# Performance work log

Measured on AMD Instinct MI355X. Metric: run time of the kernel, lower is better.

## Reference

```python
import jax, jax.numpy as jnp
import numpy as np

U, I, G = 200000, 100000, 10000
D = 64
LAYERS = 3
E_HG = 3_000_000
E_GI = 2_000_000
B = 8192


def setup_inputs() -> dict:
    key = jax.random.key(0)
    ks = jax.random.split(key, 20)
    n_hg = U + G
    n_gi = G + I
    xav = lambda k, shape: (jax.random.normal(k, shape, jnp.float32) * 0.05)
    inp = {
        "user_inputs": jax.random.randint(ks[0], (B,), 0, U),
        "pos_groups": jax.random.randint(ks[1], (B,), 0, G),
        "neg_groups": jax.random.randint(ks[2], (B,), 0, G),
        # hypergraph propagation matrix (normalized-adjacency-like values)
        "hg_rows": jax.random.randint(ks[3], (E_HG,), 0, n_hg),
        "hg_cols": jax.random.randint(ks[4], (E_HG,), 0, n_hg),
        "hg_vals": jax.random.uniform(ks[5], (E_HG,), jnp.float32) / 16.0,
        # group-item bipartite graph (one LightGCN hop)
        "gi_rows": jax.random.randint(ks[6], (E_GI,), 0, n_gi),
        "gi_cols": jax.random.randint(ks[7], (E_GI,), 0, n_gi),
        "gi_vals": jax.random.uniform(ks[8], (E_GI,), jnp.float32) / 16.0,
        # dense group-group overlap matrix
        "gg_graph": jax.random.uniform(ks[9], (G, G), jnp.float32) / float(G),
        # learned parameters
        "user_emb": xav(ks[10], (U, D)),
        "item_emb": xav(ks[11], (I, D)),
        "group_emb": xav(ks[12], (G, D)),
        "hyper_w": xav(ks[13], (D, 1)),
        "hyper_b": jnp.zeros((1,), jnp.float32),
        "lightgcn_w": xav(ks[14], (D, 1)),
        "lightgcn_b": jnp.zeros((1,), jnp.float32),
        "overlap_w": xav(ks[15], (D, 1)),
        "overlap_b": jnp.zeros((1,), jnp.float32),
    }
    return inp


def spmm(rows, cols, vals, x, n):
    # sparse(n,n) @ x : gather cols, scale, scatter-add into rows
    return jax.ops.segment_sum(vals[:, None] * x[cols], rows, num_segments=n)


def reference(user_inputs, pos_groups, neg_groups,
              hg_rows, hg_cols, hg_vals,
              gi_rows, gi_cols, gi_vals,
              gg_graph,
              user_emb, item_emb, group_emb,
              hyper_w, hyper_b, lightgcn_w, lightgcn_b, overlap_w, overlap_b):
    # --- hypergraph branch: layered SpMM + mean over (layers+1) views ---
    hg = jnp.concatenate([user_emb, group_emb], axis=0)  # [U+G, D]
    acc = hg
    cur = hg
    for _ in range(LAYERS):
        cur = spmm(hg_rows, hg_cols, hg_vals, cur, U + G)
        acc = acc + cur
    hg_mean = acc / float(LAYERS + 1)
    hg_users = hg_mean[:U]   # [U, D]
    hg_groups = hg_mean[U:]  # [G, D]

    # --- lightgcn branch: one SpMM hop over group-item graph ---
    gi = jnp.concatenate([group_emb, item_emb], axis=0)  # [G+I, D]
    gi = spmm(gi_rows, gi_cols, gi_vals, gi, G + I)
    gi_groups = gi[:G]

    # --- overlap branch: dense group-group propagation ---
    gg = gg_graph @ group_emb  # [G, D]

    # --- gated multi-view fusion ---
    sig = jax.nn.sigmoid
    hyper_coef = sig(hg_groups @ hyper_w + hyper_b)      # [G, 1]
    lightgcn_coef = sig(gi_groups @ lightgcn_w + lightgcn_b)
    overlap_coef = sig(gg @ overlap_w + overlap_b)
    groups_final = hyper_coef * hg_groups + lightgcn_coef * gi_groups + overlap_coef * gg
    users_final = hg_users

    return (users_final[user_inputs], groups_final[pos_groups], groups_final[neg_groups],
            user_emb[user_inputs], group_emb[pos_groups], group_emb[neg_groups])
```

## Files before the change

kernel.cpp:

```cpp
#include <hip/hip_runtime.h>
#include <hip/hip_bf16.h>

#define U_N 200000
#define I_N 100000
#define G_N 10000
#define B_N 8192
#define NHG (U_N + G_N)
#define GG_K 10000
#define GG_KC 313
#define GG_STRIPES 157
#define GG_SPLIT 8

#define BUCK_SHIFT 8
#define BUCK_ROWS 256
#define NBUCK 821
#define ACHUNK 12288

typedef __attribute__((ext_vector_type(8))) short bf16x8;
typedef __attribute__((ext_vector_type(4))) float f32x4;
typedef __attribute__((ext_vector_type(8))) float f32x8;
typedef __attribute__((ext_vector_type(8))) unsigned short us8;

static __device__ __forceinline__ float sigmoidf_(float x) {
    return 1.0f / (1.0f + __expf(-x));
}

static __device__ __forceinline__ unsigned bfc(float x) {
    unsigned u = __float_as_uint(x);
    return (u + 0x7fffu + ((u >> 16) & 1u)) >> 16;
}
static __device__ __forceinline__ float bsf(unsigned short u) {
    return __uint_as_float((unsigned)u << 16);
}

__global__ void k_phase1(const float* __restrict__ ge, short* __restrict__ Bfrag,
                         int* __restrict__ cursor, int cap, int bfB) {
    int bx = blockIdx.x;
    if (bx < bfB) {
        int t = bx * 256 + threadIdx.x;
        int l = t & 63;
        int ct = (t >> 6) & 3;
        int kc = t >> 8;
        int j = ct * 16 + (l & 15);
        int kb = kc * 32 + (l >> 4) * 8;
        bf16x8 pack;
#pragma unroll
        for (int e = 0; e < 8; ++e) {
            int k = kb + e;
            float f = (k < GG_K) ? ge[(size_t)k * 64 + j] : 0.f;
            pack[e] = (short)bfc(f);
        }
        *(bf16x8*)(Bfrag + (size_t)t * 8) = pack;
        return;
    }
    int b = (bx - bfB) * 256 + threadIdx.x;
    if (b < NBUCK) cursor[b] = b * cap;
}


static __device__ __forceinline__ void bscatter_body(const int* __restrict__ rows,
                                                     const int* __restrict__ cols,
                                                     const float* __restrict__ vals,
                                                     int* __restrict__ cursor,
                                                     int2* __restrict__ bpair,
                                                     int nE, int cap, int blk) {
    __shared__ int h[NBUCK];
    __shared__ int base[NBUCK];
    for (int i = threadIdx.x; i < NBUCK; i += 256) h[i] = 0;
    __syncthreads();
    int s = blk * ACHUNK;
    int end = s + ACHUNK; if (end > nE) end = nE;
    for (int e = s + threadIdx.x; e < end; e += 256)
        atomicAdd(&h[rows[e] >> BUCK_SHIFT], 1);
    __syncthreads();
    for (int i = threadIdx.x; i < NBUCK; i += 256) {
        int c = h[i];
        base[i] = c ? atomicAdd(&cursor[i], c) : 0;
        h[i] = 0;
    }
    __syncthreads();
    for (int e = s + threadIdx.x; e < end; e += 256) {
        int r = rows[e];
        int b = r >> BUCK_SHIFT;
        int pos = base[b] + atomicAdd(&h[b], 1);
        if (pos < (b + 1) * cap)
            bpair[pos] = make_int2(((r & (BUCK_ROWS - 1)) << 24) | cols[e],
                                   __float_as_int(vals[e]));
    }
}

static __device__ __forceinline__ void gg_mfma_body(const float* __restrict__ A,
                                                    const short* __restrict__ Bfrag,
                                                    float* __restrict__ part, int blk) {
    const int stripe = blk % GG_STRIPES;
    const int ks = blk / GG_STRIPES;
    const int w = threadIdx.x >> 6;
    const int l = threadIdx.x & 63;
    const int r0w = stripe * 64 + w * 16;
    int arow_i = r0w + (l & 15);
    if (arow_i > GG_K - 1) arow_i = GG_K - 1;
    const float* arow = A + (size_t)arow_i * GG_K;
    const int kg8 = (l >> 4) * 8;
    const int c0 = (ks == 0) ? 0 : 40 + 39 * (ks - 1);
    const int c1 = c0 + ((ks == 0) ? 40 : 39);
    f32x4 acc0 = {0.f, 0.f, 0.f, 0.f}, acc1 = acc0, acc2 = acc0, acc3 = acc0;
    for (int kc = c0; kc < c1; ++kc) {
        const int kbase = kc * 32 + kg8;
        bf16x8 af;
        if (kc != GG_KC - 1) {
            const float4 a0 = *(const float4*)(arow + kbase);
            const float4 a1 = *(const float4*)(arow + kbase + 4);
            af[0] = (short)bfc(a0.x); af[1] = (short)bfc(a0.y);
            af[2] = (short)bfc(a0.z); af[3] = (short)bfc(a0.w);
            af[4] = (short)bfc(a1.x); af[5] = (short)bfc(a1.y);
            af[6] = (short)bfc(a1.z); af[7] = (short)bfc(a1.w);
        } else {
#pragma unroll
            for (int e = 0; e < 8; ++e) {
                int k = kbase + e;
                af[e] = (short)bfc((k < GG_K) ? arow[k] : 0.f);
            }
        }
        const bf16x8* bp = (const bf16x8*)(Bfrag + (size_t)kc * 4 * 64 * 8);
        bf16x8 b0 = bp[0 * 64 + l];
        bf16x8 b1 = bp[1 * 64 + l];
        bf16x8 b2 = bp[2 * 64 + l];
        bf16x8 b3 = bp[3 * 64 + l];
        acc0 = __builtin_amdgcn_mfma_f32_16x16x32_bf16(af, b0, acc0, 0, 0, 0);
        acc1 = __builtin_amdgcn_mfma_f32_16x16x32_bf16(af, b1, acc1, 0, 0, 0);
        acc2 = __builtin_amdgcn_mfma_f32_16x16x32_bf16(af, b2, acc2, 0, 0, 0);
        acc3 = __builtin_amdgcn_mfma_f32_16x16x32_bf16(af, b3, acc3, 0, 0, 0);
    }
    float* po = part + (size_t)ks * GG_K * 64;
    const int orow0 = r0w + (l >> 4) * 4;
    const int ocol = l & 15;
#pragma unroll
    for (int reg = 0; reg < 4; ++reg) {
        int orow = orow0 + reg;
        if (orow < GG_K) {
            float* q = po + (size_t)orow * 64 + ocol;
            q[0]  = acc0[reg];
            q[16] = acc1[reg];
            q[32] = acc2[reg];
            q[48] = acc3[reg];
        }
    }
}

__global__ __launch_bounds__(256) void k_phase2(
    const int* __restrict__ rows, const int* __restrict__ cols,
    const float* __restrict__ vals, int* __restrict__ cursor,
    int2* __restrict__ bpair, int nE, int cap,
    const float* __restrict__ A, const short* __restrict__ Bfrag,
    float* __restrict__ part,
    const float4* __restrict__ ue4, const float4* __restrict__ ge4,
    ushort4* __restrict__ out4, const int* __restrict__ ui,
    float* __restrict__ ua, float* __restrict__ grp_acc, float* __restrict__ gi_out,
    int bsB, int ggB, int cvtB, int uaB, int gaB) {
    int bx = blockIdx.x;
    if (bx < bsB) { bscatter_body(rows, cols, vals, cursor, bpair, nE, cap, bx); return; }
    bx -= bsB;
    if (bx < ggB) { gg_mfma_body(A, Bfrag, part, bx); return; }
    bx -= ggB;
    if (bx < cvtB) {
        int i = bx * 256 + threadIdx.x;
        float4 f = (i < U_N * 16) ? ue4[i] : ge4[i - U_N * 16];
        ushort4 o;
        o.x = (unsigned short)bfc(f.x);
        o.y = (unsigned short)bfc(f.y);
        o.z = (unsigned short)bfc(f.z);
        o.w = (unsigned short)bfc(f.w);
        out4[i] = o;
        return;
    }
    bx -= cvtB;
    if (bx < uaB) {
        int idx = bx * 256 + threadIdx.x;
        int b = idx >> 6, d = idx & 63;
        ua[idx] = ((const float*)ue4)[(size_t)ui[b] * 64 + d];
        return;
    }
    bx -= uaB;
    if (bx < gaB) {
        int idx = bx * 256 + threadIdx.x;
        grp_acc[idx] = ((const float*)ge4)[idx];
        return;
    }
    bx -= gaB;
    int idx = bx * 256 + threadIdx.x;
    gi_out[idx] = 0.f;
}


static __device__ __forceinline__ void bcsr_body(const int* __restrict__ cursor,
                                                 const int2* __restrict__ bpair,
                                                 int2* __restrict__ ep,
                                                 int* __restrict__ rp, int* __restrict__ cnt,
                                                 int cap, int b) {
    __shared__ int hist[256];
    __shared__ int sc[256];
    const int tid = threadIdx.x;
    const int s = b * cap;
    int e_ = cursor[b];
    if (e_ > s + cap) e_ = s + cap;
    hist[tid] = 0;
    __syncthreads();
    for (int i = s + tid; i < e_; i += 256)
        atomicAdd(&hist[((unsigned)bpair[i].x) >> 24], 1);
    __syncthreads();
    int v = hist[tid];
    sc[tid] = v;
    __syncthreads();
    for (int off = 1; off < 256; off <<= 1) {
        int t = (tid >= off) ? sc[tid - off] : 0;
        __syncthreads();
        if (tid >= off) sc[tid] += t;
        __syncthreads();
    }
    int excl = sc[tid] - v;
    int gr = (b << BUCK_SHIFT) + tid;
    if (gr < NHG) { rp[gr] = s + excl; cnt[gr] = v; }
    hist[tid] = excl;
    __syncthreads();
    for (int i = s + tid; i < e_; i += 256) {
        int2 p = bpair[i];
        unsigned pk = (unsigned)p.x;
        int pos = atomicAdd(&hist[pk >> 24], 1);
        ep[s + pos] = make_int2((int)(pk & 0xFFFFFFu), p.y);
    }
}

static __device__ __forceinline__ void gi_body(const int* __restrict__ rows,
                                               const int* __restrict__ cols,
                                               const float* __restrict__ vals,
                                               const float* __restrict__ ge,
                                               const float* __restrict__ ie,
                                               float* __restrict__ out, int nE,
                                               int blk, int nblk) {
    int lane = threadIdx.x & 63;
    long wslot = (long)blk * 4 + (threadIdx.x >> 6);
    const long nslots = (long)nblk * 4;
    for (long base = wslot * 64; base < nE; base += nslots * 64) {
        long e = base + lane;
        int r = (e < nE) ? rows[e] : 0x7fffffff;
        bool ok = (r < G_N);
        int c = 0;
        float v = 0.f;
        if (ok) { c = cols[e]; v = vals[e]; }
        unsigned long long mask = __ballot(ok);
        while (mask) {
            int srcl = __ffsll(mask) - 1;
            mask &= mask - 1;
            int rr = __shfl(r, srcl, 64);
            int cc = __shfl(c, srcl, 64);
            float vv = __shfl(v, srcl, 64);
            const float* sp = (cc < G_N) ? (ge + (size_t)cc * 64) : (ie + (size_t)(cc - G_N) * 64);
            atomicAdd(&out[(size_t)rr * 64 + lane], vv * sp[lane]);
        }
    }
}

__global__ __launch_bounds__(256) void k_phase3(const int* __restrict__ cursor,
                                                const int2* __restrict__ bpair,
                                                int2* __restrict__ ep,
                                                int* __restrict__ rp, int* __restrict__ cnt,
                                                int cap,
                                                const int* __restrict__ grows,
                                                const int* __restrict__ gcols,
                                                const float* __restrict__ gvals,
                                                const float* __restrict__ ge,
                                                const float* __restrict__ ie,
                                                float* __restrict__ gi_out, int gnE, int giB) {
    if (blockIdx.x < NBUCK)
        bcsr_body(cursor, bpair, ep, rp, cnt, cap, blockIdx.x);
    else
        gi_body(grows, gcols, gvals, ge, ie, gi_out, gnE, blockIdx.x - NBUCK, giB);
}


static __device__ __forceinline__ void spmm_row8(const int2* __restrict__ ep, int s, int n,
                                                 const us8* __restrict__ x16,
                                                 int sub, f32x8& acc) {
#pragma unroll
    for (int t = 0; t < 8; ++t) acc[t] = 0.f;
    for (int i = 0; i < n; i += 8) {
        int2 e[8];
#pragma unroll
        for (int j = 0; j < 8; ++j) {
            int k = i + j;
            int kk = (k < n) ? k : n - 1;
            e[j] = ep[s + kk];
            if (k >= n) { e[j].y = 0; e[j].x = 0; }
        }
        us8 xv[8];
#pragma unroll
        for (int j = 0; j < 8; ++j)
            xv[j] = x16[(size_t)e[j].x * 8 + sub];
#pragma unroll
        for (int j = 0; j < 8; ++j) {
            float v = __int_as_float(e[j].y);
#pragma unroll
            for (int t = 0; t < 8; ++t) acc[t] += v * bsf(xv[j][t]);
        }
    }
}

__global__ void k_spmm8(const int* __restrict__ rp, const int* __restrict__ cnt,
                        const int2* __restrict__ ep, const us8* __restrict__ x16,
                        us8* __restrict__ out16, float* __restrict__ grp_acc,
                        const int* __restrict__ ui, float* __restrict__ usr_acc,
                        int spmmBlocks) {
    if (blockIdx.x >= spmmBlocks) {
        int idx = (blockIdx.x - spmmBlocks) * 256 + threadIdx.x;
        int b = idx >> 3, d = idx & 7;
        us8 u = x16[(size_t)ui[b] * 8 + d];
        f32x8* g = (f32x8*)usr_acc + ((size_t)b * 8 + d);
        f32x8 t = *g;
#pragma unroll
        for (int j = 0; j < 8; ++j) t[j] += bsf(u[j]);
        *g = t;
        return;
    }
    int wid = threadIdx.x >> 6;
    int lane = threadIdx.x & 63;
    int slot = lane >> 3, sub = lane & 7;
    int r = blockIdx.x * 32 + wid * 8 + slot;
    bool active = (r < NHG);
    int rr = active ? r : NHG - 1;
    int s = rp[rr];
    int n = active ? cnt[rr] : 0;
    f32x8 a;
    spmm_row8(ep, s, n, x16, sub, a);
    if (active) {
        us8 o;
#pragma unroll
        for (int j = 0; j < 8; ++j) o[j] = (unsigned short)bfc(a[j]);
        out16[(size_t)r * 8 + sub] = o;
        if (r >= U_N) {
            f32x8* g = (f32x8*)grp_acc + ((size_t)(r - U_N) * 8 + sub);
            f32x8 t = *g;
#pragma unroll
            for (int j = 0; j < 8; ++j) t[j] += a[j];
            *g = t;
        }
    }
}

__global__ void k_spmm8_final(const int* __restrict__ rp, const int* __restrict__ cnt,
                              const int2* __restrict__ ep, const us8* __restrict__ x16,
                              const int* __restrict__ ui,
                              float* __restrict__ grp_acc, float* __restrict__ usr_acc,
                              int taskBlocks) {
    if (blockIdx.x >= taskBlocks) {
        int idx = (blockIdx.x - taskBlocks) * 256 + threadIdx.x;
        int b = idx >> 3, d = idx & 7;
        us8 u = x16[(size_t)ui[b] * 8 + d];
        f32x8* g = (f32x8*)usr_acc + ((size_t)b * 8 + d);
        f32x8 t = *g;
#pragma unroll
        for (int j = 0; j < 8; ++j) t[j] += bsf(u[j]);
        *g = t;
        return;
    }
    int wid = threadIdx.x >> 6;
    int lane = threadIdx.x & 63;
    int slot = lane >> 3, sub = lane & 7;
    int t = blockIdx.x * 32 + wid * 8 + slot;
    bool active = (t < G_N + B_N);
    int tt = active ? t : 0;
    int r = (tt < G_N) ? (U_N + tt) : ui[tt - G_N];
    int s = rp[r];
    int n = active ? cnt[r] : 0;
    f32x8 a;
    spmm_row8(ep, s, n, x16, sub, a);
    if (active) {
        f32x8* g = (tt < G_N) ? ((f32x8*)grp_acc + ((size_t)tt * 8 + sub))
                              : ((f32x8*)usr_acc + ((size_t)(tt - G_N) * 8 + sub));
        f32x8 v = *g;
#pragma unroll
        for (int j = 0; j < 8; ++j) v[j] += a[j];
        *g = v;
    }
}


__global__ void k_gather_fin(const int* __restrict__ ui, const int* __restrict__ pg,
                             const int* __restrict__ ng, const float* __restrict__ ua,
                             const float* __restrict__ ga, const float* __restrict__ gi_out,
                             const float* __restrict__ gg_part,
                             const float* __restrict__ hw, const float* __restrict__ hb,
                             const float* __restrict__ lw, const float* __restrict__ lb,
                             const float* __restrict__ ow, const float* __restrict__ ob,
                             const float* __restrict__ ue, const float* __restrict__ ge,
                             float* __restrict__ out) {
    int wid = threadIdx.x >> 6, lane = threadIdx.x & 63;
    int b = blockIdx.x * 4 + wid;
    const int S = B_N * 64;
    int u = ui[b], p = pg[b], q = ng[b];
    int idx = b * 64 + lane;
    out[idx]         = ua[idx] * 0.25f;
    out[3 * S + idx] = ue[(size_t)u * 64 + lane];
    out[4 * S + idx] = ge[(size_t)p * 64 + lane];
    out[5 * S + idx] = ge[(size_t)q * 64 + lane];
    const size_t SS = (size_t)G_N * 64;
    float hwv = hw[lane], lwv = lw[lane], owv = ow[lane];
    float hb0 = hb[0], lb0 = lb[0], ob0 = ob[0];
#pragma unroll
    for (int which = 0; which < 2; ++which) {
        int g = which ? q : p;
        size_t o = (size_t)g * 64 + lane;
        float hgv = ga[o] * 0.25f;
        float giv = gi_out[o];
        float ggv = 0.f;
#pragma unroll
        for (int k = 0; k < GG_SPLIT; ++k) ggv += gg_part[k * SS + o];
        float d1 = hgv * hwv, d2 = giv * lwv, d3 = ggv * owv;
#pragma unroll
        for (int off2 = 32; off2; off2 >>= 1) {
            d1 += __shfl_xor(d1, off2, 64);
            d2 += __shfl_xor(d2, off2, 64);
            d3 += __shfl_xor(d3, off2, 64);
        }
        float val = sigmoidf_(d1 + hb0) * hgv + sigmoidf_(d2 + lb0) * giv
                  + sigmoidf_(d3 + ob0) * ggv;
        out[(which ? 2 * S : S) + idx] = val;
    }
}

extern "C" void kernel_launch(void* const* d_in, const int* in_sizes, int n_in,
                              void* d_out, int out_size, void* d_ws, size_t ws_size,
                              hipStream_t stream) {
    const int*   ui        = (const int*)d_in[0];
    const int*   pg        = (const int*)d_in[1];
    const int*   ng        = (const int*)d_in[2];
    const int*   hg_rows   = (const int*)d_in[3];
    const int*   hg_cols   = (const int*)d_in[4];
    const float* hg_vals   = (const float*)d_in[5];
    const int*   gi_rows   = (const int*)d_in[6];
    const int*   gi_cols   = (const int*)d_in[7];
    const float* gi_vals   = (const float*)d_in[8];
    const float* gg_graph  = (const float*)d_in[9];
    const float* user_emb  = (const float*)d_in[10];
    const float* item_emb  = (const float*)d_in[11];
    const float* group_emb = (const float*)d_in[12];
    const float* hyper_w   = (const float*)d_in[13];
    const float* hyper_b   = (const float*)d_in[14];
    const float* lgcn_w    = (const float*)d_in[15];
    const float* lgcn_b    = (const float*)d_in[16];
    const float* ovl_w     = (const float*)d_in[17];
    const float* ovl_b     = (const float*)d_in[18];
    const int E_HG = in_sizes[3];
    const int E_GI = in_sizes[6];

    const int nblkA = (E_HG + ACHUNK - 1) / ACHUNK;
    int cap = (E_HG + NBUCK - 1) / NBUCK;
    cap = cap + cap / 4 + 64;
    cap = (cap + 63) & ~63;

    char* ws = (char*)d_ws;
    size_t off = 0;
    auto alloc = [&](size_t bytes) -> char* {
        char* p = ws + off;
        off += (bytes + 255) & ~(size_t)255;
        return p;
    };
    int*   cursor  = (int*)alloc((size_t)NBUCK * 4);
    int2*  bpair   = (int2*)alloc((size_t)NBUCK * cap * 8);
    int2*  ep      = (int2*)alloc((size_t)NBUCK * cap * 8 + 1024);
    int*   rp      = (int*)alloc((size_t)NHG * 4);
    int*   cnt     = (int*)alloc((size_t)NHG * 4);
    __hip_bfloat16* curA = (__hip_bfloat16*)alloc((size_t)NHG * 64 * 2);
    __hip_bfloat16* curB = (__hip_bfloat16*)alloc((size_t)NHG * 64 * 2);
    float* grp_acc = (float*)alloc((size_t)G_N * 64 * 4);
    float* gi_out  = (float*)alloc((size_t)G_N * 64 * 4);
    float* usr_acc = (float*)alloc((size_t)B_N * 64 * 4);
    short* Bfrag   = (short*)alloc((size_t)GG_KC * 4 * 64 * 8 * 2);
    float* gg_part = (float*)alloc((size_t)GG_SPLIT * GG_K * 64 * 4);
    (void)ws_size; (void)n_in; (void)out_size;

    k_phase1<<<GG_KC + 4, 256, 0, stream>>>(group_emb, Bfrag, cursor, cap, GG_KC);

    const int ggB  = GG_STRIPES * GG_SPLIT;
    const int cvtB = (NHG * 16) / 256;
    const int uaB  = (B_N * 64) / 256;
    const int gaB  = (G_N * 64) / 256;
    const int gzB  = (G_N * 64) / 256;
    k_phase2<<<nblkA + ggB + cvtB + uaB + gaB + gzB, 256, 0, stream>>>(
        hg_rows, hg_cols, hg_vals, cursor, bpair, E_HG, cap,
        gg_graph, Bfrag, gg_part,
        (const float4*)user_emb, (const float4*)group_emb, (ushort4*)curB, ui,
        usr_acc, grp_acc, gi_out, nblkA, ggB, cvtB, uaB, gaB);

    const int giB = 2048;
    k_phase3<<<NBUCK + giB, 256, 0, stream>>>(cursor, bpair, ep, rp, cnt, cap,
                                              gi_rows, gi_cols, gi_vals,
                                              group_emb, item_emb, gi_out, E_GI, giB);

    const int spmmB = (NHG + 31) / 32;
    const int uaExt = (B_N * 8) / 256;

    k_spmm8<<<spmmB, 256, 0, stream>>>(rp, cnt, ep, (const us8*)curB,
                                       (us8*)curA, grp_acc, nullptr, nullptr, spmmB);
    k_spmm8<<<spmmB + uaExt, 256, 0, stream>>>(rp, cnt, ep, (const us8*)curA,
                                               (us8*)curB, grp_acc, ui, usr_acc, spmmB);
    const int taskB = (G_N + B_N + 31) / 32;
    k_spmm8_final<<<taskB + uaExt, 256, 0, stream>>>(rp, cnt, ep, (const us8*)curB, ui,
                                                     grp_acc, usr_acc, taskB);

    k_gather_fin<<<B_N / 4, 256, 0, stream>>>(ui, pg, ng, usr_acc, grp_acc, gi_out, gg_part,
                                              hyper_w, hyper_b, lgcn_w, lgcn_b, ovl_w, ovl_b,
                                              user_emb, group_emb, (float*)d_out);
}
```

Before: 416.9 us.

## Replace atomic bucket cursors with per-block histogram plus global exclusive scan

```diff
diff --git a/kernel.cpp b/kernel.cpp
--- a/kernel.cpp
+++ b/kernel.cpp
@@ -33,59 +33,110 @@
     return __uint_as_float((unsigned)u << 16);
 }
 
-__global__ void k_phase1(const float* __restrict__ ge, short* __restrict__ Bfrag,
-                         int* __restrict__ cursor, int cap, int bfB) {
+
+__global__ void k_scan_partial(const int* __restrict__ in, int* __restrict__ out,
+                               int* __restrict__ bsums, int n) {
+    __shared__ int sh[256];
+    int tid = threadIdx.x;
+    int base = blockIdx.x * 1024 + tid * 4;
+    int v0 = (base + 0 < n) ? in[base + 0] : 0;
+    int v1 = (base + 1 < n) ? in[base + 1] : 0;
+    int v2 = (base + 2 < n) ? in[base + 2] : 0;
+    int v3 = (base + 3 < n) ? in[base + 3] : 0;
+    int s = v0 + v1 + v2 + v3;
+    sh[tid] = s;
+    __syncthreads();
+    for (int off = 1; off < 256; off <<= 1) {
+        int t = (tid >= off) ? sh[tid - off] : 0;
+        __syncthreads();
+        if (tid >= off) sh[tid] += t;
+        __syncthreads();
+    }
+    int excl = sh[tid] - s;
+    if (tid == 255) bsums[blockIdx.x] = sh[255];
+    if (base + 0 < n) out[base + 0] = excl; excl += v0;
+    if (base + 1 < n) out[base + 1] = excl; excl += v1;
+    if (base + 2 < n) out[base + 2] = excl; excl += v2;
+    if (base + 3 < n) out[base + 3] = excl;
+}
+
+__global__ void k_scan_sums(int* bsums, int nb) {
+    __shared__ int sh[256];
+    int tid = threadIdx.x;
+    int v = (tid < nb) ? bsums[tid] : 0;
+    sh[tid] = v;
+    __syncthreads();
+    for (int off = 1; off < 256; off <<= 1) {
+        int t = (tid >= off) ? sh[tid - off] : 0;
+        __syncthreads();
+        if (tid >= off) sh[tid] += t;
+        __syncthreads();
+    }
+    if (tid < nb) bsums[tid] = sh[tid] - v;
+}
+
+__global__ void k_scan_add(int* out, const int* __restrict__ bsums, int n) {
+    int base = blockIdx.x * 1024 + threadIdx.x * 4;
+    int add = bsums[blockIdx.x];
+#pragma unroll
+    for (int j = 0; j < 4; ++j)
+        if (base + j < n) out[base + j] += add;
+}
+
+__global__ void k_phase1(const int* __restrict__ rows, int* __restrict__ M,
+                         int nE, int nblk,
+                         const float* __restrict__ ge, short* __restrict__ Bfrag,
+                         int bhB) {
     int bx = blockIdx.x;
-    if (bx < bfB) {
-        int t = bx * 256 + threadIdx.x;
-        int l = t & 63;
-        int ct = (t >> 6) & 3;
-        int kc = t >> 8;
-        int j = ct * 16 + (l & 15);
-        int kb = kc * 32 + (l >> 4) * 8;
-        bf16x8 pack;
-#pragma unroll
-        for (int e = 0; e < 8; ++e) {
-            int k = kb + e;
-            float f = (k < GG_K) ? ge[(size_t)k * 64 + j] : 0.f;
-            pack[e] = (short)bfc(f);
-        }
-        *(bf16x8*)(Bfrag + (size_t)t * 8) = pack;
+    if (bx < bhB) {
+        __shared__ int h[NBUCK];
+        for (int i = threadIdx.x; i < NBUCK; i += 256) h[i] = 0;
+        __syncthreads();
+        int s = bx * ACHUNK;
+        int end = s + ACHUNK; if (end > nE) end = nE;
+        for (int e = s + threadIdx.x; e < end; e += 256)
+            atomicAdd(&h[rows[e] >> BUCK_SHIFT], 1);
+        __syncthreads();
+        for (int b = threadIdx.x; b < NBUCK; b += 256)
+            M[(size_t)b * nblk + bx] = h[b];
         return;
     }
-    int b = (bx - bfB) * 256 + threadIdx.x;
-    if (b < NBUCK) cursor[b] = b * cap;
+    bx -= bhB;
+    int t = bx * 256 + threadIdx.x;
+    int l = t & 63;
+    int ct = (t >> 6) & 3;
+    int kc = t >> 8;
+    int j = ct * 16 + (l & 15);
+    int kb = kc * 32 + (l >> 4) * 8;
+    bf16x8 pack;
+#pragma unroll
+    for (int e = 0; e < 8; ++e) {
+        int k = kb + e;
+        float f = (k < GG_K) ? ge[(size_t)k * 64 + j] : 0.f;
+        pack[e] = (short)bfc(f);
+    }
+    *(bf16x8*)(Bfrag + (size_t)t * 8) = pack;
 }
 
 
 static __device__ __forceinline__ void bscatter_body(const int* __restrict__ rows,
                                                      const int* __restrict__ cols,
                                                      const float* __restrict__ vals,
-                                                     int* __restrict__ cursor,
+                                                     const int* __restrict__ M,
                                                      int2* __restrict__ bpair,
-                                                     int nE, int cap, int blk) {
-    __shared__ int h[NBUCK];
+                                                     int nE, int nblk, int blk) {
     __shared__ int base[NBUCK];
-    for (int i = threadIdx.x; i < NBUCK; i += 256) h[i] = 0;
+    for (int i = threadIdx.x; i < NBUCK; i += 256)
+        base[i] = M[(size_t)i * nblk + blk];
     __syncthreads();
     int s = blk * ACHUNK;
     int end = s + ACHUNK; if (end > nE) end = nE;
-    for (int e = s + threadIdx.x; e < end; e += 256)
-        atomicAdd(&h[rows[e] >> BUCK_SHIFT], 1);
-    __syncthreads();
-    for (int i = threadIdx.x; i < NBUCK; i += 256) {
-        int c = h[i];
-        base[i] = c ? atomicAdd(&cursor[i], c) : 0;
-        h[i] = 0;
-    }
-    __syncthreads();
     for (int e = s + threadIdx.x; e < end; e += 256) {
         int r = rows[e];
         int b = r >> BUCK_SHIFT;
-        int pos = base[b] + atomicAdd(&h[b], 1);
-        if (pos < (b + 1) * cap)
-            bpair[pos] = make_int2(((r & (BUCK_ROWS - 1)) << 24) | cols[e],
-                                   __float_as_int(vals[e]));
+        int pos = atomicAdd(&base[b], 1);
+        bpair[pos] = make_int2(((r & (BUCK_ROWS - 1)) << 24) | cols[e],
+                               __float_as_int(vals[e]));
     }
 }
 
@@ -149,8 +200,8 @@
 
 __global__ __launch_bounds__(256) void k_phase2(
     const int* __restrict__ rows, const int* __restrict__ cols,
-    const float* __restrict__ vals, int* __restrict__ cursor,
-    int2* __restrict__ bpair, int nE, int cap,
+    const float* __restrict__ vals, const int* __restrict__ M,
+    int2* __restrict__ bpair, int nE, int nblk,
     const float* __restrict__ A, const short* __restrict__ Bfrag,
     float* __restrict__ part,
     const float4* __restrict__ ue4, const float4* __restrict__ ge4,
@@ -158,7 +209,7 @@
     float* __restrict__ ua, float* __restrict__ grp_acc, float* __restrict__ gi_out,
     int bsB, int ggB, int cvtB, int uaB, int gaB) {
     int bx = blockIdx.x;
-    if (bx < bsB) { bscatter_body(rows, cols, vals, cursor, bpair, nE, cap, bx); return; }
+    if (bx < bsB) { bscatter_body(rows, cols, vals, M, bpair, nE, nblk, bx); return; }
     bx -= bsB;
     if (bx < ggB) { gg_mfma_body(A, Bfrag, part, bx); return; }
     bx -= ggB;
@@ -192,17 +243,16 @@
 }
 
 
-static __device__ __forceinline__ void bcsr_body(const int* __restrict__ cursor,
+static __device__ __forceinline__ void bcsr_body(const int* __restrict__ M, int nblk,
                                                  const int2* __restrict__ bpair,
                                                  int2* __restrict__ ep,
                                                  int* __restrict__ rp, int* __restrict__ cnt,
-                                                 int cap, int b) {
+                                                 int nE, int b) {
     __shared__ int hist[256];
     __shared__ int sc[256];
     const int tid = threadIdx.x;
-    const int s = b * cap;
-    int e_ = cursor[b];
-    if (e_ > s + cap) e_ = s + cap;
+    const int s = M[(size_t)b * nblk];
+    const int e_ = (b + 1 < NBUCK) ? M[(size_t)(b + 1) * nblk] : nE;
     hist[tid] = 0;
     __syncthreads();
     for (int i = s + tid; i < e_; i += 256)
@@ -260,11 +310,11 @@
     }
 }
 
-__global__ __launch_bounds__(256) void k_phase3(const int* __restrict__ cursor,
+__global__ __launch_bounds__(256) void k_phase3(const int* __restrict__ M, int nblk,
                                                 const int2* __restrict__ bpair,
                                                 int2* __restrict__ ep,
                                                 int* __restrict__ rp, int* __restrict__ cnt,
-                                                int cap,
+                                                int nE,
                                                 const int* __restrict__ grows,
                                                 const int* __restrict__ gcols,
                                                 const float* __restrict__ gvals,
@@ -272,7 +322,7 @@
                                                 const float* __restrict__ ie,
                                                 float* __restrict__ gi_out, int gnE, int giB) {
     if (blockIdx.x < NBUCK)
-        bcsr_body(cursor, bpair, ep, rp, cnt, cap, blockIdx.x);
+        bcsr_body(M, nblk, bpair, ep, rp, cnt, nE, blockIdx.x);
     else
         gi_body(grows, gcols, gvals, ge, ie, gi_out, gnE, blockIdx.x - NBUCK, giB);
 }
@@ -453,9 +503,8 @@
     const int E_GI = in_sizes[6];
 
     const int nblkA = (E_HG + ACHUNK - 1) / ACHUNK;
-    int cap = (E_HG + NBUCK - 1) / NBUCK;
-    cap = cap + cap / 4 + 64;
-    cap = (cap + 63) & ~63;
+    const int nM = NBUCK * nblkA;
+    const int nbM = (nM + 1023) / 1024;
 
     char* ws = (char*)d_ws;
     size_t off = 0;
@@ -464,9 +513,10 @@
         off += (bytes + 255) & ~(size_t)255;
         return p;
     };
-    int*   cursor  = (int*)alloc((size_t)NBUCK * 4);
-    int2*  bpair   = (int2*)alloc((size_t)NBUCK * cap * 8);
-    int2*  ep      = (int2*)alloc((size_t)NBUCK * cap * 8 + 1024);
+    int*   M       = (int*)alloc((size_t)nM * 4);
+    int*   bsums   = (int*)alloc(256 * 4);
+    int2*  bpair   = (int2*)alloc((size_t)E_HG * 8);
+    int2*  ep      = (int2*)alloc((size_t)E_HG * 8 + 1024);
     int*   rp      = (int*)alloc((size_t)NHG * 4);
     int*   cnt     = (int*)alloc((size_t)NHG * 4);
     __hip_bfloat16* curA = (__hip_bfloat16*)alloc((size_t)NHG * 64 * 2);
@@ -478,7 +528,11 @@
     float* gg_part = (float*)alloc((size_t)GG_SPLIT * GG_K * 64 * 4);
     (void)ws_size; (void)n_in; (void)out_size;
 
-    k_phase1<<<GG_KC + 4, 256, 0, stream>>>(group_emb, Bfrag, cursor, cap, GG_KC);
+    k_phase1<<<nblkA + GG_KC, 256, 0, stream>>>(hg_rows, M, E_HG, nblkA,
+                                                group_emb, Bfrag, nblkA);
+    k_scan_partial<<<nbM, 256, 0, stream>>>(M, M, bsums, nM);
+    k_scan_sums<<<1, 256, 0, stream>>>(bsums, nbM);
+    k_scan_add<<<nbM, 256, 0, stream>>>(M, bsums, nM);
 
     const int ggB  = GG_STRIPES * GG_SPLIT;
     const int cvtB = (NHG * 16) / 256;
@@ -486,13 +540,13 @@
     const int gaB  = (G_N * 64) / 256;
     const int gzB  = (G_N * 64) / 256;
     k_phase2<<<nblkA + ggB + cvtB + uaB + gaB + gzB, 256, 0, stream>>>(
-        hg_rows, hg_cols, hg_vals, cursor, bpair, E_HG, cap,
+        hg_rows, hg_cols, hg_vals, M, bpair, E_HG, nblkA,
         gg_graph, Bfrag, gg_part,
         (const float4*)user_emb, (const float4*)group_emb, (ushort4*)curB, ui,
         usr_acc, grp_acc, gi_out, nblkA, ggB, cvtB, uaB, gaB);
 
     const int giB = 2048;
-    k_phase3<<<NBUCK + giB, 256, 0, stream>>>(cursor, bpair, ep, rp, cnt, cap,
+    k_phase3<<<NBUCK + giB, 256, 0, stream>>>(M, nblkA, bpair, ep, rp, cnt, E_HG,
                                               gi_rows, gi_cols, gi_vals,
                                               group_emb, item_emb, gi_out, E_GI, giB);
 
```

Measured after the change: 437.8 us. 5.0% more time.
